# Performance work log

Hardware: AMD Instinct MI355X
Metric: run time of the kernel (lower is better)

Reference implementation:

```python
import jax, jax.numpy as jnp
import numpy as np

C = 256
CQK = C // 8  # 32

def setup_inputs() -> dict:
    key = jax.random.key(0)
    ks = jax.random.split(key, 8)
    x = jax.random.normal(ks[0], (4, C, 64, 64), dtype=jnp.float32)
    Wq = jax.random.normal(ks[1], (CQK, C), dtype=jnp.float32) * 0.02
    bq = jnp.zeros((CQK,), dtype=jnp.float32)
    Wk = jax.random.normal(ks[2], (CQK, C), dtype=jnp.float32) * 0.02
    bk = jnp.zeros((CQK,), dtype=jnp.float32)
    Wv = jax.random.normal(ks[3], (C, C), dtype=jnp.float32) * 0.02
    bv = jnp.zeros((C,), dtype=jnp.float32)
    # torch init: gamma = zeros(1); use small nonzero so backward path through attention is exercised? -> stay faithful: zeros
    gamma = jnp.zeros((1,), dtype=jnp.float32)
    return {"x": x, "Wq": Wq, "bq": bq, "Wk": Wk, "bk": bk, "Wv": Wv, "bv": bv, "gamma": gamma}


def reference(x, Wq, bq, Wk, bk, Wv, bv, gamma):
    B, Cc, H, W = x.shape
    N = H * W
    xf = x.reshape(B, Cc, N)                              # B,C,N
    # 1x1 convs == per-position matmuls
    q = jnp.einsum('bcn,dc->bnd', xf, Wq) + bq            # B,N,C/8  (proj_query permuted)
    k = jnp.einsum('bcn,dc->bdn', xf, Wk) + bk[:, None]   # B,C/8,N
    v = jnp.einsum('bcn,dc->bdn', xf, Wv) + bv[:, None]   # B,C,N
    energy = jnp.einsum('bnd,bdm->bnm', q, k)             # B,N,N
    attention = jax.nn.softmax(energy, axis=-1)           # softmax over last dim
    # out[b,c,m] = sum_n v[b,c,n] * attention[b,m,n]
    out = jnp.einsum('bcn,bmn->bcm', v, attention)
    out = out.reshape(B, Cc, H, W)
    return gamma * out + x
```

## Files before the change

### kernel.cpp

```cpp
#include <hip/hip_runtime.h>

#define B_  4
#define N_  4096
#define C_  256
#define D_  32

typedef __attribute__((ext_vector_type(8))) short bf8;
typedef __attribute__((ext_vector_type(4))) float f4;

__device__ __forceinline__ unsigned short bft(float f) {
    unsigned u = __builtin_bit_cast(unsigned, f);
    return (unsigned short)((u + 0x8000u) >> 16);
}
__device__ __forceinline__ unsigned pk2(float a, float b) {
    unsigned ua = __builtin_bit_cast(unsigned, a) + 0x8000u;
    unsigned ub = __builtin_bit_cast(unsigned, b) + 0x8000u;
    return __builtin_amdgcn_perm(ub, ua, 0x07060302u);
}

__global__ __launch_bounds__(256) void prep(
    const float* __restrict__ Wq, const float* __restrict__ Wk,
    const float* __restrict__ Wv,
    unsigned short* __restrict__ Wqkb, unsigned short* __restrict__ Wvb)
{
    int i = blockIdx.x * 256 + threadIdx.x;
    if (i < 8192)       Wqkb[i] = bft(Wq[i]);
    else if (i < 16384) Wqkb[i] = bft(Wk[i - 8192]);
    Wvb[i] = bft(Wv[i]);
}

__global__ __launch_bounds__(256) void qkv(
    const float* __restrict__ x,
    const unsigned short* __restrict__ Wqkb, const unsigned short* __restrict__ Wvb,
    const float* __restrict__ bq, const float* __restrict__ bk,
    const float* __restrict__ bv,
    unsigned short* __restrict__ qb, unsigned short* __restrict__ kb,
    unsigned short* __restrict__ vb)
{
    const int b = blockIdx.y, n0 = blockIdx.x * 32;
    const int t = threadIdx.x;
    const int lane = t & 63, w = t >> 6, c15 = lane & 15, g = lane >> 4;

    __shared__ __align__(16) unsigned short xs[32][264];

    {
        const int r = t >> 3, cg = t & 7;
        #pragma unroll
        for (int it = 0; it < 8; ++it) {
            int c = r + 32 * it;
            float4 v = *(const float4*)(x + ((size_t)(b * C_ + c)) * N_ + n0 + cg * 4);
            xs[cg * 4 + 0][c] = bft(v.x);
            xs[cg * 4 + 1][c] = bft(v.y);
            xs[cg * 4 + 2][c] = bft(v.z);
            xs[cg * 4 + 3][c] = bft(v.w);
        }
    }
    __syncthreads();

    f4 qkacc[2]; f4 vacc[2][4];
    const f4 fz = {0.f, 0.f, 0.f, 0.f};
    qkacc[0] = fz; qkacc[1] = fz;
    #pragma unroll
    for (int nt = 0; nt < 2; ++nt)
        #pragma unroll
        for (int ct = 0; ct < 4; ++ct) vacc[nt][ct] = fz;

    const unsigned short* wqk = Wqkb + (w * 16 + c15) * C_ + g * 8;
    const unsigned short* wv0 = Wvb + (w * 64 + c15) * C_ + g * 8;
    const unsigned short* xsp = &xs[c15][g * 8];

    #pragma unroll
    for (int ks = 0; ks < 8; ++ks) {
        bf8 xf0 = *(const bf8*)(xsp + ks * 32);
        bf8 xf1 = *(const bf8*)(xsp + 16 * 264 + ks * 32);
        bf8 af  = *(const bf8*)(wqk + ks * 32);
        qkacc[0] = __builtin_amdgcn_mfma_f32_16x16x32_bf16(af, xf0, qkacc[0], 0, 0, 0);
        qkacc[1] = __builtin_amdgcn_mfma_f32_16x16x32_bf16(af, xf1, qkacc[1], 0, 0, 0);
        #pragma unroll
        for (int ct = 0; ct < 4; ++ct) {
            bf8 bfv = *(const bf8*)(wv0 + ct * 16 * C_ + ks * 32);
            vacc[0][ct] = __builtin_amdgcn_mfma_f32_16x16x32_bf16(xf0, bfv, vacc[0][ct], 0, 0, 0);
            vacc[1][ct] = __builtin_amdgcn_mfma_f32_16x16x32_bf16(xf1, bfv, vacc[1][ct], 0, 0, 0);
        }
    }

    {
        float4 bias = (w < 2) ? *(const float4*)(bq + (w & 1) * 16 + 4 * g)
                              : *(const float4*)(bk + (w & 1) * 16 + 4 * g);
        float sc = (w < 2) ? 1.44269504f : 1.0f;
        unsigned short* base = (w < 2) ? qb : kb;
        int d0 = (w & 1) * 16 + 4 * g;
        #pragma unroll
        for (int nt = 0; nt < 2; ++nt) {
            int n = n0 + nt * 16 + c15;
            f4 a = qkacc[nt];
            uint2 pk;
            pk.x = pk2((a.x + bias.x) * sc, (a.y + bias.y) * sc);
            pk.y = pk2((a.z + bias.z) * sc, (a.w + bias.w) * sc);
            *(uint2*)(base + ((size_t)(b * N_ + n)) * D_ + d0) = pk;
        }
    }
    #pragma unroll
    for (int ct = 0; ct < 4; ++ct) {
        int cout = w * 64 + ct * 16 + c15;
        float bvv = bv[cout];
        #pragma unroll
        for (int nt = 0; nt < 2; ++nt) {
            f4 a = vacc[nt][ct];
            uint2 pk;
            pk.x = pk2(a.x + bvv, a.y + bvv);
            pk.y = pk2(a.z + bvv, a.w + bvv);
            *(uint2*)(vb + ((size_t)(b * C_ + cout)) * (size_t)N_ + n0 + nt * 16 + 4 * g) = pk;
        }
    }
}

__global__ __launch_bounds__(512, 2) void attn(
    const unsigned short* __restrict__ qb, const unsigned short* __restrict__ kb,
    const unsigned short* __restrict__ vb, const float* __restrict__ x,
    const float* __restrict__ gamma, float* __restrict__ out)
{
    const int b = blockIdx.z, c0 = blockIdx.y * 128, m0 = blockIdx.x * 128;
    const int t = threadIdx.x;
    const int lane = t & 63, w = t >> 6, c15 = lane & 15, g = lane >> 4;
    const int pm = w & 3, ph = w >> 2;
    const int mtg = w & 1, ctg = (w >> 1) & 1, ksh = w >> 2;

    __shared__ __align__(16) unsigned short Ps[2][128][136];
    __shared__ float l_s[2][128];

    const f4 fz = {0.f, 0.f, 0.f, 0.f};

    bf8 qf[2];
    #pragma unroll
    for (int mi = 0; mi < 2; ++mi)
        qf[mi] = *(const bf8*)(qb + ((size_t)(b * N_ + m0 + (2 * pm + mi) * 16 + c15)) * D_ + g * 8);

    bf8 kf[4];
    #pragma unroll
    for (int ff = 0; ff < 4; ++ff)
        kf[ff] = *(const bf8*)(kb + ((size_t)(b * N_ + (ph * 4 + ff) * 16 + c15)) * D_ + g * 8);

    f4 acc[4][4];
    #pragma unroll
    for (int mt = 0; mt < 4; ++mt)
        #pragma unroll
        for (int ct = 0; ct < 4; ++ct) acc[mt][ct] = fz;
    float lrun[2] = {0.f, 0.f};

    const unsigned short* vbase = vb + ((size_t)(b * C_ + c0 + ctg * 64)) * (size_t)N_;

    for (int j0 = 0; j0 < N_; j0 += 128) {
        const int buf = (j0 >> 7) & 1;
        bf8 vf[2][4];
        #pragma unroll
        for (int ki = 0; ki < 2; ++ki)
            #pragma unroll
            for (int ct = 0; ct < 4; ++ct)
                vf[ki][ct] = *(const bf8*)(vbase + (size_t)(ct * 16 + c15) * N_
                                           + j0 + (ksh * 2 + ki) * 32 + g * 8);
        f4 s[2][4];
        #pragma unroll
        for (int mi = 0; mi < 2; ++mi)
            #pragma unroll
            for (int ff = 0; ff < 4; ++ff)
                s[mi][ff] = __builtin_amdgcn_mfma_f32_16x16x32_bf16(kf[ff], qf[mi], fz, 0, 0, 0);
        if (j0 + 128 < N_) {
            #pragma unroll
            for (int ff = 0; ff < 4; ++ff)
                kf[ff] = *(const bf8*)(kb + ((size_t)(b * N_ + j0 + 128 + (ph * 4 + ff) * 16 + c15)) * D_ + g * 8);
        }
        #pragma unroll
        for (int mi = 0; mi < 2; ++mi) {
            #pragma unroll
            for (int ff = 0; ff < 4; ++ff) {
                float p0 = __builtin_amdgcn_exp2f(s[mi][ff].x);
                float p1 = __builtin_amdgcn_exp2f(s[mi][ff].y);
                float p2 = __builtin_amdgcn_exp2f(s[mi][ff].z);
                float p3 = __builtin_amdgcn_exp2f(s[mi][ff].w);
                lrun[mi] += (p0 + p1) + (p2 + p3);
                uint2 pk; pk.x = pk2(p0, p1); pk.y = pk2(p2, p3);
                *(uint2*)&Ps[buf][(2 * pm + mi) * 16 + c15][(ph * 4 + ff) * 16 + 4 * g] = pk;
            }
        }
        asm volatile("s_waitcnt lgkmcnt(0)\n\ts_barrier" ::: "memory");
        #pragma unroll
        for (int ki = 0; ki < 2; ++ki) {
            const int kcol = (ksh * 2 + ki) * 32 + g * 8;
            bf8 pf[4];
            #pragma unroll
            for (int mt = 0; mt < 4; ++mt)
                pf[mt] = *(const bf8*)&Ps[buf][(mtg * 4 + mt) * 16 + c15][kcol];
            #pragma unroll
            for (int mt = 0; mt < 4; ++mt)
                #pragma unroll
                for (int ct = 0; ct < 4; ++ct)
                    acc[mt][ct] = __builtin_amdgcn_mfma_f32_16x16x32_bf16(pf[mt], vf[ki][ct], acc[mt][ct], 0, 0, 0);
        }
    }

    #pragma unroll
    for (int mi = 0; mi < 2; ++mi) {
        lrun[mi] += __shfl_xor(lrun[mi], 16);
        lrun[mi] += __shfl_xor(lrun[mi], 32);
    }
    if (lane < 16) {
        l_s[ph][(2 * pm) * 16 + lane]     = lrun[0];
        l_s[ph][(2 * pm + 1) * 16 + lane] = lrun[1];
    }
    __syncthreads();

    float* accs = (float*)&Ps[0][0][0];
    const int pos = w & 3;
    if (ksh == 1) {
        #pragma unroll
        for (int mt = 0; mt < 4; ++mt)
            #pragma unroll
            for (int ct = 0; ct < 4; ++ct)
                *(f4*)&accs[(((pos * 16 + mt * 4 + ct) * 64) + lane) * 4] = acc[mt][ct];
    }
    __syncthreads();
    if (ksh == 0) {
        const float g0 = gamma[0];
        #pragma unroll
        for (int mt = 0; mt < 4; ++mt) {
            const int mrow = (mtg * 4 + mt) * 16;
            float4 la = *(const float4*)&l_s[0][mrow + 4 * g];
            float4 lb = *(const float4*)&l_s[1][mrow + 4 * g];
            float i0 = 1.f / (la.x + lb.x), i1 = 1.f / (la.y + lb.y);
            float i2 = 1.f / (la.z + lb.z), i3 = 1.f / (la.w + lb.w);
            #pragma unroll
            for (int ct = 0; ct < 4; ++ct) {
                f4 o = *(const f4*)&accs[(((pos * 16 + mt * 4 + ct) * 64) + lane) * 4];
                f4 a = acc[mt][ct];
                int c = c0 + (ctg * 4 + ct) * 16 + c15;
                size_t base = ((size_t)(b * C_ + c)) * (size_t)N_ + m0 + mrow + 4 * g;
                float4 xv = *(const float4*)(x + base);
                float4 r;
                r.x = g0 * ((a.x + o.x) * i0) + xv.x;
                r.y = g0 * ((a.y + o.y) * i1) + xv.y;
                r.z = g0 * ((a.z + o.z) * i2) + xv.z;
                r.w = g0 * ((a.w + o.w) * i3) + xv.w;
                *(float4*)(out + base) = r;
            }
        }
    }
}

extern "C" void kernel_launch(void* const* d_in, const int* in_sizes, int n_in,
                              void* d_out, int out_size, void* d_ws, size_t ws_size,
                              hipStream_t stream) {
    const float* x     = (const float*)d_in[0];
    const float* Wq    = (const float*)d_in[1];
    const float* bq    = (const float*)d_in[2];
    const float* Wk    = (const float*)d_in[3];
    const float* bk    = (const float*)d_in[4];
    const float* Wv    = (const float*)d_in[5];
    const float* bv    = (const float*)d_in[6];
    const float* gamma = (const float*)d_in[7];
    float* out = (float*)d_out;

    unsigned short* qb   = (unsigned short*)d_ws;
    unsigned short* kb   = qb + (size_t)B_ * N_ * D_;
    unsigned short* vb   = kb + (size_t)B_ * N_ * D_;
    unsigned short* Wqkb = vb + (size_t)B_ * C_ * N_;
    unsigned short* Wvb  = Wqkb + 64 * C_;

    prep<<<256, 256, 0, stream>>>(Wq, Wk, Wv, Wqkb, Wvb);
    qkv<<<dim3(128, 4), 256, 0, stream>>>(x, Wqkb, Wvb, bq, bk, bv, qb, kb, vb);
    attn<<<dim3(32, 2, 4), 512, 0, stream>>>(qb, kb, vb, x, gamma, out);
}
```

Before: 173.2 us.

## Double wave count per block in attention and QKV kernels, shrink per-wave tiles

The attention kernel moves from 8 to 16 waves per block, so each wave owns one query tile for the scores and a 32x64 output tile instead of 64x64. Per-wave accumulator registers drop, which is meant to raise latency hiding and the number of waves in flight. The QKV kernel likewise uses 512 threads over 64 positions. In exchange, each barrier now has more waves to synchronise, V fragments are loaded redundantly by more waves, and the launch-bounds hint of four 1024-thread blocks per CU may not be achievable.

Result: slower. 242.1 us (+39.8%).

```diff
diff --git a/kernel.cpp b/kernel.cpp
--- a/kernel.cpp
+++ b/kernel.cpp
@@ -29,7 +29,7 @@
     Wvb[i] = bft(Wv[i]);
 }
 
-__global__ __launch_bounds__(256) void qkv(
+__global__ __launch_bounds__(512) void qkv(
     const float* __restrict__ x,
     const unsigned short* __restrict__ Wqkb, const unsigned short* __restrict__ Wvb,
     const float* __restrict__ bq, const float* __restrict__ bk,
@@ -37,23 +37,22 @@
     unsigned short* __restrict__ qb, unsigned short* __restrict__ kb,
     unsigned short* __restrict__ vb)
 {
-    const int b = blockIdx.y, n0 = blockIdx.x * 32;
+    const int b = blockIdx.y, n0 = blockIdx.x * 64;
     const int t = threadIdx.x;
     const int lane = t & 63, w = t >> 6, c15 = lane & 15, g = lane >> 4;
-
-    __shared__ __align__(16) unsigned short xs[32][264];
-
-    {
-        const int r = t >> 3, cg = t & 7;
-        #pragma unroll
-        for (int it = 0; it < 8; ++it) {
-            int c = r + 32 * it;
-            float4 v = *(const float4*)(x + ((size_t)(b * C_ + c)) * N_ + n0 + cg * 4);
-            xs[cg * 4 + 0][c] = bft(v.x);
-            xs[cg * 4 + 1][c] = bft(v.y);
-            xs[cg * 4 + 2][c] = bft(v.z);
-            xs[cg * 4 + 3][c] = bft(v.w);
-        }
+    const int vr = w & 3, nh = w >> 2;
+
+    __shared__ __align__(16) unsigned short xs[64][264];
+
+    #pragma unroll
+    for (int it = 0; it < 8; ++it) {
+        int idx = t + 512 * it;
+        int c = idx >> 4, q = idx & 15;
+        float4 v = *(const float4*)(x + ((size_t)(b * C_ + c)) * N_ + n0 + q * 4);
+        xs[q * 4 + 0][c] = bft(v.x);
+        xs[q * 4 + 1][c] = bft(v.y);
+        xs[q * 4 + 2][c] = bft(v.z);
+        xs[q * 4 + 3][c] = bft(v.w);
     }
     __syncthreads();
 
@@ -65,9 +64,9 @@
         #pragma unroll
         for (int ct = 0; ct < 4; ++ct) vacc[nt][ct] = fz;
 
-    const unsigned short* wqk = Wqkb + (w * 16 + c15) * C_ + g * 8;
-    const unsigned short* wv0 = Wvb + (w * 64 + c15) * C_ + g * 8;
-    const unsigned short* xsp = &xs[c15][g * 8];
+    const unsigned short* wqk = Wqkb + (vr * 16 + c15) * C_ + g * 8;
+    const unsigned short* wv0 = Wvb + (vr * 64 + c15) * C_ + g * 8;
+    const unsigned short* xsp = &xs[nh * 32 + c15][g * 8];
 
     #pragma unroll
     for (int ks = 0; ks < 8; ++ks) {
@@ -85,14 +84,14 @@
     }
 
     {
-        float4 bias = (w < 2) ? *(const float4*)(bq + (w & 1) * 16 + 4 * g)
-                              : *(const float4*)(bk + (w & 1) * 16 + 4 * g);
-        float sc = (w < 2) ? 1.44269504f : 1.0f;
-        unsigned short* base = (w < 2) ? qb : kb;
-        int d0 = (w & 1) * 16 + 4 * g;
+        float4 bias = (vr < 2) ? *(const float4*)(bq + (vr & 1) * 16 + 4 * g)
+                               : *(const float4*)(bk + (vr & 1) * 16 + 4 * g);
+        float sc = (vr < 2) ? 1.44269504f : 1.0f;
+        unsigned short* base = (vr < 2) ? qb : kb;
+        int d0 = (vr & 1) * 16 + 4 * g;
         #pragma unroll
         for (int nt = 0; nt < 2; ++nt) {
-            int n = n0 + nt * 16 + c15;
+            int n = n0 + (nh * 2 + nt) * 16 + c15;
             f4 a = qkacc[nt];
             uint2 pk;
             pk.x = pk2((a.x + bias.x) * sc, (a.y + bias.y) * sc);
@@ -102,7 +101,7 @@
     }
     #pragma unroll
     for (int ct = 0; ct < 4; ++ct) {
-        int cout = w * 64 + ct * 16 + c15;
+        int cout = vr * 64 + ct * 16 + c15;
         float bvv = bv[cout];
         #pragma unroll
         for (int nt = 0; nt < 2; ++nt) {
@@ -110,12 +109,13 @@
             uint2 pk;
             pk.x = pk2(a.x + bvv, a.y + bvv);
             pk.y = pk2(a.z + bvv, a.w + bvv);
-            *(uint2*)(vb + ((size_t)(b * C_ + cout)) * (size_t)N_ + n0 + nt * 16 + 4 * g) = pk;
-        }
-    }
-}
-
-__global__ __launch_bounds__(512, 2) void attn(
+            *(uint2*)(vb + ((size_t)(b * C_ + cout)) * (size_t)N_
+                      + n0 + (nh * 2 + nt) * 16 + 4 * g) = pk;
+        }
+    }
+}
+
+__global__ __launch_bounds__(1024, 4) void attn(
     const unsigned short* __restrict__ qb, const unsigned short* __restrict__ kb,
     const unsigned short* __restrict__ vb, const float* __restrict__ x,
     const float* __restrict__ gamma, float* __restrict__ out)
@@ -123,117 +123,104 @@
     const int b = blockIdx.z, c0 = blockIdx.y * 128, m0 = blockIdx.x * 128;
     const int t = threadIdx.x;
     const int lane = t & 63, w = t >> 6, c15 = lane & 15, g = lane >> 4;
-    const int pm = w & 3, ph = w >> 2;
-    const int mtg = w & 1, ctg = (w >> 1) & 1, ksh = w >> 2;
+    const int pm = w & 7, pnh = w >> 3;
+    const int mq = w & 3, cq = (w >> 2) & 1, ksh = w >> 3;
 
     __shared__ __align__(16) unsigned short Ps[2][128][136];
     __shared__ float l_s[2][128];
 
     const f4 fz = {0.f, 0.f, 0.f, 0.f};
 
-    bf8 qf[2];
+    bf8 qf = *(const bf8*)(qb + ((size_t)(b * N_ + m0 + pm * 16 + c15)) * D_ + g * 8);
+
+    const unsigned short* kptr = kb + ((size_t)(b * N_ + pnh * 64 + c15)) * D_ + g * 8;
+    bf8 kf[4];
+    #pragma unroll
+    for (int ff = 0; ff < 4; ++ff)
+        kf[ff] = *(const bf8*)(kptr + (size_t)ff * 16 * D_);
+    kptr += (size_t)128 * D_;
+
+    f4 acc[2][4];
     #pragma unroll
     for (int mi = 0; mi < 2; ++mi)
-        qf[mi] = *(const bf8*)(qb + ((size_t)(b * N_ + m0 + (2 * pm + mi) * 16 + c15)) * D_ + g * 8);
-
-    bf8 kf[4];
-    #pragma unroll
-    for (int ff = 0; ff < 4; ++ff)
-        kf[ff] = *(const bf8*)(kb + ((size_t)(b * N_ + (ph * 4 + ff) * 16 + c15)) * D_ + g * 8);
-
-    f4 acc[4][4];
-    #pragma unroll
-    for (int mt = 0; mt < 4; ++mt)
-        #pragma unroll
-        for (int ct = 0; ct < 4; ++ct) acc[mt][ct] = fz;
-    float lrun[2] = {0.f, 0.f};
-
-    const unsigned short* vbase = vb + ((size_t)(b * C_ + c0 + ctg * 64)) * (size_t)N_;
-
-    for (int j0 = 0; j0 < N_; j0 += 128) {
-        const int buf = (j0 >> 7) & 1;
+        #pragma unroll
+        for (int ct = 0; ct < 4; ++ct) acc[mi][ct] = fz;
+    float lrun = 0.f;
+
+    const unsigned short* vptr = vb + ((size_t)(b * C_ + c0 + cq * 64)) * (size_t)N_
+                                 + ksh * 64 + g * 8;
+
+    for (int it = 0; it < 32; ++it) {
+        const int buf = it & 1;
         bf8 vf[2][4];
         #pragma unroll
         for (int ki = 0; ki < 2; ++ki)
             #pragma unroll
             for (int ct = 0; ct < 4; ++ct)
-                vf[ki][ct] = *(const bf8*)(vbase + (size_t)(ct * 16 + c15) * N_
-                                           + j0 + (ksh * 2 + ki) * 32 + g * 8);
-        f4 s[2][4];
+                vf[ki][ct] = *(const bf8*)(vptr + (size_t)(ct * 16 + c15) * N_ + ki * 32);
+        f4 s[4];
+        #pragma unroll
+        for (int ff = 0; ff < 4; ++ff)
+            s[ff] = __builtin_amdgcn_mfma_f32_16x16x32_bf16(kf[ff], qf, fz, 0, 0, 0);
+        if (it < 31) {
+            #pragma unroll
+            for (int ff = 0; ff < 4; ++ff)
+                kf[ff] = *(const bf8*)(kptr + (size_t)ff * 16 * D_);
+            kptr += (size_t)128 * D_;
+        }
+        #pragma unroll
+        for (int ff = 0; ff < 4; ++ff) {
+            float p0 = __builtin_amdgcn_exp2f(s[ff].x);
+            float p1 = __builtin_amdgcn_exp2f(s[ff].y);
+            float p2 = __builtin_amdgcn_exp2f(s[ff].z);
+            float p3 = __builtin_amdgcn_exp2f(s[ff].w);
+            lrun += (p0 + p1) + (p2 + p3);
+            uint2 pk; pk.x = pk2(p0, p1); pk.y = pk2(p2, p3);
+            *(uint2*)&Ps[buf][pm * 16 + c15][(pnh * 4 + ff) * 16 + 4 * g] = pk;
+        }
+        asm volatile("s_waitcnt lgkmcnt(0)\n\ts_barrier" ::: "memory");
+        #pragma unroll
+        for (int ki = 0; ki < 2; ++ki) {
+            const int kcol = ksh * 64 + ki * 32 + g * 8;
+            bf8 pf0 = *(const bf8*)&Ps[buf][(2 * mq + 0) * 16 + c15][kcol];
+            bf8 pf1 = *(const bf8*)&Ps[buf][(2 * mq + 1) * 16 + c15][kcol];
+            #pragma unroll
+            for (int ct = 0; ct < 4; ++ct) {
+                acc[0][ct] = __builtin_amdgcn_mfma_f32_16x16x32_bf16(pf0, vf[ki][ct], acc[0][ct], 0, 0, 0);
+                acc[1][ct] = __builtin_amdgcn_mfma_f32_16x16x32_bf16(pf1, vf[ki][ct], acc[1][ct], 0, 0, 0);
+            }
+        }
+        vptr += 128;
+    }
+
+    lrun += __shfl_xor(lrun, 16);
+    lrun += __shfl_xor(lrun, 32);
+    if (lane < 16) l_s[pnh][pm * 16 + lane] = lrun;
+    __syncthreads();
+
+    float* accs = (float*)&Ps[0][0][0];
+    if (ksh == 1) {
         #pragma unroll
         for (int mi = 0; mi < 2; ++mi)
             #pragma unroll
-            for (int ff = 0; ff < 4; ++ff)
-                s[mi][ff] = __builtin_amdgcn_mfma_f32_16x16x32_bf16(kf[ff], qf[mi], fz, 0, 0, 0);
-        if (j0 + 128 < N_) {
-            #pragma unroll
-            for (int ff = 0; ff < 4; ++ff)
-                kf[ff] = *(const bf8*)(kb + ((size_t)(b * N_ + j0 + 128 + (ph * 4 + ff) * 16 + c15)) * D_ + g * 8);
-        }
-        #pragma unroll
-        for (int mi = 0; mi < 2; ++mi) {
-            #pragma unroll
-            for (int ff = 0; ff < 4; ++ff) {
-                float p0 = __builtin_amdgcn_exp2f(s[mi][ff].x);
-                float p1 = __builtin_amdgcn_exp2f(s[mi][ff].y);
-                float p2 = __builtin_amdgcn_exp2f(s[mi][ff].z);
-                float p3 = __builtin_amdgcn_exp2f(s[mi][ff].w);
-                lrun[mi] += (p0 + p1) + (p2 + p3);
-                uint2 pk; pk.x = pk2(p0, p1); pk.y = pk2(p2, p3);
-                *(uint2*)&Ps[buf][(2 * pm + mi) * 16 + c15][(ph * 4 + ff) * 16 + 4 * g] = pk;
-            }
-        }
-        asm volatile("s_waitcnt lgkmcnt(0)\n\ts_barrier" ::: "memory");
-        #pragma unroll
-        for (int ki = 0; ki < 2; ++ki) {
-            const int kcol = (ksh * 2 + ki) * 32 + g * 8;
-            bf8 pf[4];
-            #pragma unroll
-            for (int mt = 0; mt < 4; ++mt)
-                pf[mt] = *(const bf8*)&Ps[buf][(mtg * 4 + mt) * 16 + c15][kcol];
-            #pragma unroll
-            for (int mt = 0; mt < 4; ++mt)
-                #pragma unroll
-                for (int ct = 0; ct < 4; ++ct)
-                    acc[mt][ct] = __builtin_amdgcn_mfma_f32_16x16x32_bf16(pf[mt], vf[ki][ct], acc[mt][ct], 0, 0, 0);
-        }
-    }
-
-    #pragma unroll
-    for (int mi = 0; mi < 2; ++mi) {
-        lrun[mi] += __shfl_xor(lrun[mi], 16);
-        lrun[mi] += __shfl_xor(lrun[mi], 32);
-    }
-    if (lane < 16) {
-        l_s[ph][(2 * pm) * 16 + lane]     = lrun[0];
-        l_s[ph][(2 * pm + 1) * 16 + lane] = lrun[1];
-    }
-    __syncthreads();
-
-    float* accs = (float*)&Ps[0][0][0];
-    const int pos = w & 3;
-    if (ksh == 1) {
-        #pragma unroll
-        for (int mt = 0; mt < 4; ++mt)
-            #pragma unroll
             for (int ct = 0; ct < 4; ++ct)
-                *(f4*)&accs[(((pos * 16 + mt * 4 + ct) * 64) + lane) * 4] = acc[mt][ct];
+                *(f4*)&accs[(((w & 7) * 8 + mi * 4 + ct) * 64 + lane) * 4] = acc[mi][ct];
     }
     __syncthreads();
     if (ksh == 0) {
         const float g0 = gamma[0];
         #pragma unroll
-        for (int mt = 0; mt < 4; ++mt) {
-            const int mrow = (mtg * 4 + mt) * 16;
+        for (int mi = 0; mi < 2; ++mi) {
+            const int mrow = (2 * mq + mi) * 16;
             float4 la = *(const float4*)&l_s[0][mrow + 4 * g];
             float4 lb = *(const float4*)&l_s[1][mrow + 4 * g];
             float i0 = 1.f / (la.x + lb.x), i1 = 1.f / (la.y + lb.y);
             float i2 = 1.f / (la.z + lb.z), i3 = 1.f / (la.w + lb.w);
             #pragma unroll
             for (int ct = 0; ct < 4; ++ct) {
-                f4 o = *(const f4*)&accs[(((pos * 16 + mt * 4 + ct) * 64) + lane) * 4];
-                f4 a = acc[mt][ct];
-                int c = c0 + (ctg * 4 + ct) * 16 + c15;
+                f4 o = *(const f4*)&accs[((w * 8 + mi * 4 + ct) * 64 + lane) * 4];
+                f4 a = acc[mi][ct];
+                int c = c0 + (cq * 4 + ct) * 16 + c15;
                 size_t base = ((size_t)(b * C_ + c)) * (size_t)N_ + m0 + mrow + 4 * g;
                 float4 xv = *(const float4*)(x + base);
                 float4 r;
@@ -267,6 +254,6 @@
     unsigned short* Wvb  = Wqkb + 64 * C_;
 
     prep<<<256, 256, 0, stream>>>(Wq, Wk, Wv, Wqkb, Wvb);
-    qkv<<<dim3(128, 4), 256, 0, stream>>>(x, Wqkb, Wvb, bq, bk, bv, qb, kb, vb);
-    attn<<<dim3(32, 2, 4), 512, 0, stream>>>(qb, kb, vb, x, gamma, out);
-}
+    qkv<<<dim3(64, 4), 512, 0, stream>>>(x, Wqkb, Wvb, bq, bk, bv, qb, kb, vb);
+    attn<<<dim3(32, 2, 4), 1024, 0, stream>>>(qb, kb, vb, x, gamma, out);
+}
```
